# Performance work log

Hardware: AMD Instinct MI355X
Metric: run time of the kernel (lower is better)

Reference implementation:

```python
import jax, jax.numpy as jnp
import numpy as np
import math

H, NH, DH, FF = 768, 12, 64, 3072
B, S = 8, 1024

def _gelu(x):
    return x * 0.5 * (1.0 + jax.lax.erf(x / math.sqrt(2.0)))

def _layernorm(x, gamma, beta, eps=1e-6):
    mean = jnp.mean(x, axis=-1, keepdims=True)
    std = jnp.std(x, axis=-1, keepdims=True, ddof=1)  # torch unbiased std
    return gamma * (x - mean) / (std + eps) + beta

def setup_inputs() -> dict:
    key = jax.random.key(0)
    ks = jax.random.split(key, 16)
    p = lambda k, shape: jax.random.normal(k, shape, dtype=jnp.float32) * 0.02
    return {
        "hidden": jax.random.normal(ks[0], (B, S, H), dtype=jnp.float32),
        "mask": jnp.zeros((B, 1, S, S), dtype=jnp.float32),
        "position_bias": jax.random.normal(ks[1], (1, NH, S, S), dtype=jnp.float32),
        "Wq": p(ks[2], (H, H)), "bq": jnp.zeros((H,), jnp.float32),
        "Wk": p(ks[3], (H, H)), "bk": jnp.zeros((H,), jnp.float32),
        "Wv": p(ks[4], (H, H)), "bv": jnp.zeros((H,), jnp.float32),
        "Wo": p(ks[5], (H, H)), "bo": jnp.zeros((H,), jnp.float32),
        "W1": p(ks[6], (H, FF)), "b1": jnp.zeros((FF,), jnp.float32),
        "W2": p(ks[7], (FF, H)), "b2": jnp.zeros((H,), jnp.float32),
        "g1": jnp.ones((H,), jnp.float32), "beta1": jnp.zeros((H,), jnp.float32),
        "g2": jnp.ones((H,), jnp.float32), "beta2": jnp.zeros((H,), jnp.float32),
    }

def reference(hidden, mask, position_bias, Wq, bq, Wk, bk, Wv, bv, Wo, bo,
              W1, b1, W2, b2, g1, beta1, g2, beta2):
    b, s, _ = hidden.shape
    def split_heads(x):
        return x.reshape(b, s, NH, DH).transpose(0, 2, 1, 3)  # [b, h, s, d]
    q = split_heads(hidden @ Wq + bq)
    k = split_heads(hidden @ Wk + bk)
    v = split_heads(hidden @ Wv + bv)
    scores = jnp.einsum('bhqd,bhkd->bhqk', q, k)
    scores = scores + position_bias          # bias added BEFORE scaling (as in source)
    scores = scores / math.sqrt(float(DH))
    scores = scores + mask
    probs = jax.nn.softmax(scores, axis=-1)  # dropout is identity in eval
    ctx = jnp.einsum('bhqk,bhkd->bhqd', probs, v)
    ctx = ctx.transpose(0, 2, 1, 3).reshape(b, s, NH * DH)
    attn_out = ctx @ Wo + bo
    inter = _layernorm(attn_out + hidden, g1, beta1)
    ffn = _gelu(inter @ W1 + b1) @ W2 + b2
    return _layernorm(ffn + inter, g2, beta2)
```

## Files before the change

### kernel.cpp

```cpp
#include <hip/hip_runtime.h>
#include <cmath>

typedef __bf16 bf16;
typedef __attribute__((ext_vector_type(8))) __bf16 bf16x8;
typedef __attribute__((ext_vector_type(4))) __bf16 bf16x4;
typedef __attribute__((ext_vector_type(4))) float f32x4;

#define DEVINL __device__ __forceinline__

DEVINL void gload16(const void* g, void* l) {
    __builtin_amdgcn_global_load_lds((const __attribute__((address_space(1))) void*)g,
                                     (__attribute__((address_space(3))) void*)l, 16, 0, 0);
}


__global__ void cast_bf16_kernel(const float* __restrict__ in, bf16* __restrict__ out, int n4) {
    int i = blockIdx.x * 256 + threadIdx.x;
    if (i < n4) {
        float4 v = ((const float4*)in)[i];
        bf16x4 o;
        o[0] = (bf16)v.x; o[1] = (bf16)v.y; o[2] = (bf16)v.z; o[3] = (bf16)v.w;
        ((bf16x4*)out)[i] = o;
    }
}

__global__ void prep_pm_kernel(const float* __restrict__ pb, const float* __restrict__ mask,
                               bf16* __restrict__ pbs, bf16* __restrict__ maskb,
                               int n1, int n2) {
    const int i = blockIdx.x * 256 + threadIdx.x;
    const float c1 = 0.18033688011112042f;
    const float c2 = 1.4426950408889634f;
    if (i < n1) {
        float4 v = ((const float4*)pb)[i];
        bf16x4 o;
        o[0] = (bf16)(v.x * c1); o[1] = (bf16)(v.y * c1);
        o[2] = (bf16)(v.z * c1); o[3] = (bf16)(v.w * c1);
        ((bf16x4*)pbs)[i] = o;
    } else if (i < n1 + n2) {
        const int j = i - n1;
        float4 v = ((const float4*)mask)[j];
        bf16x4 o;
        o[0] = (bf16)(v.x * c2); o[1] = (bf16)(v.y * c2);
        o[2] = (bf16)(v.z * c2); o[3] = (bf16)(v.w * c2);
        ((bf16x4*)maskb)[j] = o;
    }
}

__global__ void tcast_kernel(const float* __restrict__ in, bf16* __restrict__ out, int R, int C) {
    __shared__ float t[32][33];
    int tx = threadIdx.x & 31, ty = threadIdx.x >> 5;
    int r0 = blockIdx.y * 32, c0 = blockIdx.x * 32;
#pragma unroll
    for (int i = 0; i < 4; ++i)
        t[ty + 8 * i][tx] = in[(size_t)(r0 + ty + 8 * i) * C + c0 + tx];
    __syncthreads();
#pragma unroll
    for (int i = 0; i < 4; ++i)
        out[(size_t)(c0 + ty + 8 * i) * R + r0 + tx] = (bf16)t[tx][ty + 8 * i];
}

__global__ void concat_bias_kernel(const float* __restrict__ a, const float* __restrict__ b,
                                   const float* __restrict__ c, float* __restrict__ out) {
    int i = blockIdx.x * 256 + threadIdx.x;
    if (i < 2304) out[i] = (i < 768) ? a[i] : ((i < 1536) ? b[i - 768] : c[i - 1536]);
}

__global__ __launch_bounds__(256) void vtrans_kernel(const bf16* __restrict__ qkv,
                                                     bf16* __restrict__ vT) {
    __shared__ bf16 t[64][72];
    const int tid = threadIdx.x;
    const int bh = blockIdx.y, s0 = blockIdx.x * 32;
    const int b = bh / 12, h = bh % 12;
    {
        const int r = tid >> 3, c8 = (tid & 7) * 8;
        bf16x8 v = *(const bf16x8*)(qkv + (size_t)(b * 1024 + s0 + r) * 2304 + 1536 + h * 64 + c8);
#pragma unroll
        for (int j = 0; j < 8; ++j) t[c8 + j][r] = v[j];
    }
    __syncthreads();
    {
        const int d = tid >> 2, s8 = (tid & 3) * 8;
        bf16x8 o = *(const bf16x8*)(&t[d][s8]);
        *(bf16x8*)(vT + (size_t)(bh * 64 + d) * 1024 + s0 + s8) = o;
    }
}

template<int MODE, int BN>
__global__ __launch_bounds__(256, 4) void gemm_kernel(const bf16* __restrict__ A, const bf16* __restrict__ Bt,
                                                      const float* __restrict__ bias,
                                                      bf16* __restrict__ Cb,
                                                      int M, int N, int K, int ldc) {
    constexpr int NI = BN / 32;
    constexpr int BLOADS = BN / 32;
    __shared__ __align__(16) bf16 As[128 * 64];
    __shared__ __align__(16) bf16 Bs[BN * 64];
    const int tid = threadIdx.x;
    const int wid = tid >> 6, lane = tid & 63;
    const int L = blockIdx.y * gridDim.x + blockIdx.x;
    const int cpx = (gridDim.x * gridDim.y) >> 3;
    const int wg = (L & 7) * cpx + (L >> 3);
    const int m0 = (wg / gridDim.x) * 128, n0 = (wg % gridDim.x) * BN;
    const int wr = (wid >> 1) * 64, wc = (wid & 1) * (BN / 2);
    const int lg = lane >> 4, l15 = lane & 15;
    f32x4 acc[4][NI] = {};

    for (int k0 = 0; k0 < K; k0 += 64) {
        __syncthreads();
#pragma unroll
        for (int i = 0; i < 4; ++i) {
            const int cbase = (wid * 4 + i) * 1024;
            const int td = cbase + lane * 16;
            const int row = td >> 7;
            const int s16 = ((td >> 4) & 7) ^ (row & 7);
            gload16(A + (size_t)(m0 + row) * K + k0 + s16 * 8, (char*)As + cbase);
        }
#pragma unroll
        for (int i = 0; i < BLOADS; ++i) {
            const int cbase = (wid * BLOADS + i) * 1024;
            const int td = cbase + lane * 16;
            const int row = td >> 7;
            const int s16 = ((td >> 4) & 7) ^ (row & 7);
            gload16(Bt + (size_t)(n0 + row) * K + k0 + s16 * 8, (char*)Bs + cbase);
        }
        __syncthreads();
#pragma unroll
        for (int kk = 0; kk < 2; ++kk) {
            bf16x8 af[4], bfr[NI];
#pragma unroll
            for (int mi = 0; mi < 4; ++mi) {
                int ra = wr + mi * 16 + l15;
                int off = (ra * 128 + (kk * 32 + 8 * lg) * 2) ^ ((ra & 7) << 4);
                af[mi] = *(const bf16x8*)((const char*)As + off);
            }
#pragma unroll
            for (int ni = 0; ni < NI; ++ni) {
                int rb = wc + ni * 16 + l15;
                int off = (rb * 128 + (kk * 32 + 8 * lg) * 2) ^ ((rb & 7) << 4);
                bfr[ni] = *(const bf16x8*)((const char*)Bs + off);
            }
#pragma unroll
            for (int mi = 0; mi < 4; ++mi)
#pragma unroll
                for (int ni = 0; ni < NI; ++ni)
                    acc[mi][ni] = __builtin_amdgcn_mfma_f32_16x16x32_bf16(af[mi], bfr[ni], acc[mi][ni], 0, 0, 0);
        }
    }
#pragma unroll
    for (int mi = 0; mi < 4; ++mi) {
#pragma unroll
        for (int r = 0; r < 4; ++r) {
            const int row = m0 + wr + mi * 16 + lg * 4 + r;
#pragma unroll
            for (int ni = 0; ni < NI; ++ni) {
                const int col = n0 + wc + ni * 16 + l15;
                float v = acc[mi][ni][r] + bias[col];
                if (MODE == 2) v = v * 0.5f * (1.0f + erff(v * 0.70710678118654752f));
                Cb[(size_t)row * ldc + col] = (bf16)v;
            }
        }
    }
}

__global__ __launch_bounds__(256, 3) void attn_kernel(const bf16* __restrict__ qkv,
                                                      const bf16* __restrict__ pbs,
                                                      const bf16* __restrict__ maskb,
                                                      const bf16* __restrict__ vT,
                                                      bf16* __restrict__ ctx) {
    __shared__ __align__(16) bf16 Kb[3][64 * 64];
    __shared__ __align__(16) bf16 Vb[3][64 * 64];
    const int tid = threadIdx.x, wid = tid >> 6, lane = tid & 63;
    const int bh = blockIdx.y, b = bh / 12, h = bh % 12;
    const int q0 = blockIdx.x * 128 + wid * 32;
    const int lg = lane >> 4, l15 = lane & 15;
    const float cqk = 0.18033688011112042f;

    bf16x8 aq[2][2];
#pragma unroll
    for (int qs = 0; qs < 2; ++qs) {
        const size_t r = (size_t)(b * 1024 + q0 + qs * 16 + l15) * 2304 + h * 64 + 8 * lg;
        aq[qs][0] = *(const bf16x8*)(qkv + r);
        aq[qs][1] = *(const bf16x8*)(qkv + r + 32);
    }

    auto stage = [&](int tt, int pp) {
#pragma unroll
        for (int rd = 0; rd < 2; ++rd) {
            const int n = rd * 256 + tid;
            const int i = n >> 3, sl = n & 7, c = sl ^ (i & 7);
            const int sig = (i & 32) | ((i & 12) << 1) | ((i & 16) >> 2) | (i & 3);
            gload16(qkv + (size_t)(b * 1024 + tt * 64 + sig) * 2304 + 768 + h * 64 + c * 8,
                    (char*)Kb[pp] + (rd * 256 + wid * 64) * 16);
            gload16(vT + ((size_t)bh * 64 + i) * 1024 + tt * 64 + c * 8,
                    (char*)Vb[pp] + (rd * 256 + wid * 64) * 16);
        }
    };

    float mrun[2] = {-1e30f, -1e30f}, lsum[2] = {0.f, 0.f};
    f32x4 acc[2][4] = {};

    stage(0, 0);
    stage(1, 1);
    __syncthreads();
    for (int t = 0; t < 16; ++t) {
        const int p = t % 3;
        const int k0 = t * 64;
        bf16x8 pbv[2][2], mkv[2][2];
#pragma unroll
        for (int qs = 0; qs < 2; ++qs) {
            const int q = q0 + qs * 16 + l15;
            const bf16* pr = pbs + ((size_t)h * 1024 + q) * 1024 + k0 + lg * 8;
            const bf16* mr = maskb + ((size_t)b * 1024 + q) * 1024 + k0 + lg * 8;
            pbv[qs][0] = *(const bf16x8*)pr;  pbv[qs][1] = *(const bf16x8*)(pr + 32);
            mkv[qs][0] = *(const bf16x8*)mr;  mkv[qs][1] = *(const bf16x8*)(mr + 32);
        }
        if (t < 14) stage(t + 2, (t + 2) % 3);

        bf16x8 bk[4][2];
#pragma unroll
        for (int kt = 0; kt < 4; ++kt) {
            const int row = kt * 16 + l15;
            const int byte = (row * 128 + lg * 16) ^ ((row & 7) << 4);
            bk[kt][0] = *(const bf16x8*)((const char*)Kb[p] + byte);
            bk[kt][1] = *(const bf16x8*)((const char*)Kb[p] + (byte ^ 64));
        }
        f32x4 s[2][4];
#pragma unroll
        for (int qs = 0; qs < 2; ++qs)
#pragma unroll
            for (int kt = 0; kt < 4; ++kt) {
                f32x4 z = {};
                z = __builtin_amdgcn_mfma_f32_16x16x32_bf16(bk[kt][0], aq[qs][0], z, 0, 0, 0);
                z = __builtin_amdgcn_mfma_f32_16x16x32_bf16(bk[kt][1], aq[qs][1], z, 0, 0, 0);
                s[qs][kt] = z;
            }
#pragma unroll
        for (int qs = 0; qs < 2; ++qs)
#pragma unroll
            for (int kt = 0; kt < 4; ++kt)
#pragma unroll
                for (int r = 0; r < 4; ++r) {
                    const int j = (kt & 1) * 4 + r;
                    s[qs][kt][r] = s[qs][kt][r] * cqk
                                 + (float)pbv[qs][kt >> 1][j]
                                 + (float)mkv[qs][kt >> 1][j];
                }
        bf16x8 po[2][2];
#pragma unroll
        for (int qs = 0; qs < 2; ++qs) {
            float tm = s[qs][0][0];
#pragma unroll
            for (int kt = 0; kt < 4; ++kt)
#pragma unroll
                for (int r = 0; r < 4; ++r) tm = fmaxf(tm, s[qs][kt][r]);
            tm = fmaxf(tm, __shfl_xor(tm, 16));
            tm = fmaxf(tm, __shfl_xor(tm, 32));
            if (!__all(tm <= mrun[qs] + 6.0f)) {
                const float mn = fmaxf(mrun[qs], tm);
                const float scal = __builtin_amdgcn_exp2f(mrun[qs] - mn);
                mrun[qs] = mn;
                lsum[qs] *= scal;
#pragma unroll
                for (int dt = 0; dt < 4; ++dt) {
                    acc[qs][dt][0] *= scal; acc[qs][dt][1] *= scal;
                    acc[qs][dt][2] *= scal; acc[qs][dt][3] *= scal;
                }
            }
            float ts = 0.f;
#pragma unroll
            for (int kt = 0; kt < 4; ++kt)
#pragma unroll
                for (int r = 0; r < 4; ++r) {
                    const float pv = __builtin_amdgcn_exp2f(s[qs][kt][r] - mrun[qs]);
                    ts += pv;
                    const int idx = kt * 4 + r;
                    if (idx < 8) po[qs][0][idx] = (bf16)pv;
                    else         po[qs][1][idx - 8] = (bf16)pv;
                }
            ts += __shfl_xor(ts, 16);
            ts += __shfl_xor(ts, 32);
            lsum[qs] += ts;
        }
        bf16x8 vb[4][2];
#pragma unroll
        for (int dt = 0; dt < 4; ++dt) {
            const int row = dt * 16 + l15;
            const int byte = (row * 128 + lg * 16) ^ ((row & 7) << 4);
            vb[dt][0] = *(const bf16x8*)((const char*)Vb[p] + byte);
            vb[dt][1] = *(const bf16x8*)((const char*)Vb[p] + (byte ^ 64));
        }
#pragma unroll
        for (int qs = 0; qs < 2; ++qs)
#pragma unroll
            for (int dt = 0; dt < 4; ++dt) {
                acc[qs][dt] = __builtin_amdgcn_mfma_f32_16x16x32_bf16(vb[dt][0], po[qs][0], acc[qs][dt], 0, 0, 0);
                acc[qs][dt] = __builtin_amdgcn_mfma_f32_16x16x32_bf16(vb[dt][1], po[qs][1], acc[qs][dt], 0, 0, 0);
            }
        __syncthreads();
    }
    char* scr = (char*)Kb + wid * 4096;
#pragma unroll
    for (int qs = 0; qs < 2; ++qs) {
        const float inv = 1.0f / lsum[qs];
        const int ql = qs * 16 + l15;
#pragma unroll
        for (int dt = 0; dt < 4; ++dt) {
            bf16x4 o;
#pragma unroll
            for (int r = 0; r < 4; ++r) o[r] = (bf16)(acc[qs][dt][r] * inv);
            const int wb = (ql * 128 + dt * 32 + lg * 8) ^ ((ql & 7) << 4);
            *(bf16x4*)(scr + wb) = o;
        }
    }
    __syncthreads();
#pragma unroll
    for (int qs = 0; qs < 2; ++qs) {
        const int ql = qs * 16 + l15;
        const int rb = (ql * 128 + lg * 32) ^ ((ql & 7) << 4);
        bf16x8 o0 = *(const bf16x8*)(scr + rb);
        bf16x8 o1 = *(const bf16x8*)(scr + (rb ^ 16));
        bf16* cp = ctx + (size_t)(b * 1024 + q0 + ql) * 768 + h * 64 + lg * 16;
        *(bf16x8*)cp = o0;
        *(bf16x8*)(cp + 8) = o1;
    }
}

template<int MODE>
__global__ __launch_bounds__(256) void ln_kernel(const bf16* __restrict__ xb,
                                                 const float* __restrict__ resf,
                                                 const bf16* __restrict__ resb,
                                                 const float* __restrict__ g, const float* __restrict__ bt,
                                                 float* __restrict__ outf, bf16* __restrict__ outb) {
    const int wid = threadIdx.x >> 6, lane = threadIdx.x & 63;
    const int row = blockIdx.x * 4 + wid;
    float4 v[3];
    float s = 0.f, ss = 0.f;
#pragma unroll
    for (int j = 0; j < 3; ++j) {
        bf16x4 xa = ((const bf16x4*)(xb + (size_t)row * 768))[lane + 64 * j];
        float4 b;
        if (MODE == 0) {
            b = ((const float4*)(resf + (size_t)row * 768))[lane + 64 * j];
        } else {
            bf16x4 rb = ((const bf16x4*)(resb + (size_t)row * 768))[lane + 64 * j];
            b.x = (float)rb[0]; b.y = (float)rb[1]; b.z = (float)rb[2]; b.w = (float)rb[3];
        }
        float4 w;
        w.x = (float)xa[0] + b.x; w.y = (float)xa[1] + b.y;
        w.z = (float)xa[2] + b.z; w.w = (float)xa[3] + b.w;
        v[j] = w;
        s += w.x + w.y + w.z + w.w;
        ss += w.x * w.x + w.y * w.y + w.z * w.z + w.w * w.w;
    }
#pragma unroll
    for (int off = 1; off <= 32; off <<= 1) { s += __shfl_xor(s, off); ss += __shfl_xor(ss, off); }
    const float mean = s * (1.f / 768.f);
    float var = (ss - 768.f * mean * mean) * (1.f / 767.f);
    var = fmaxf(var, 0.f);
    const float inv = 1.f / (sqrtf(var) + 1e-6f);
#pragma unroll
    for (int j = 0; j < 3; ++j) {
        float4 gv = ((const float4*)g)[lane + 64 * j];
        float4 bv = ((const float4*)bt)[lane + 64 * j];
        float4 y;
        y.x = gv.x * (v[j].x - mean) * inv + bv.x;
        y.y = gv.y * (v[j].y - mean) * inv + bv.y;
        y.z = gv.z * (v[j].z - mean) * inv + bv.z;
        y.w = gv.w * (v[j].w - mean) * inv + bv.w;
        if (MODE == 1) {
            ((float4*)(outf + (size_t)row * 768))[lane + 64 * j] = y;
        } else {
            bf16x4 o;
            o[0] = (bf16)y.x; o[1] = (bf16)y.y; o[2] = (bf16)y.z; o[3] = (bf16)y.w;
            ((bf16x4*)(outb + (size_t)row * 768))[lane + 64 * j] = o;
        }
    }
}


extern "C" void kernel_launch(void* const* d_in, const int* in_sizes, int n_in,
                              void* d_out, int out_size, void* d_ws, size_t ws_size,
                              hipStream_t stream) {
    const float* hidden = (const float*)d_in[0];
    const float* mask   = (const float*)d_in[1];
    const float* pb     = (const float*)d_in[2];
    const float* Wq = (const float*)d_in[3];
    const float* bq = (const float*)d_in[4];
    const float* Wk = (const float*)d_in[5];
    const float* bk = (const float*)d_in[6];
    const float* Wv = (const float*)d_in[7];
    const float* bv = (const float*)d_in[8];
    const float* Wo = (const float*)d_in[9];
    const float* bo = (const float*)d_in[10];
    const float* W1 = (const float*)d_in[11];
    const float* b1 = (const float*)d_in[12];
    const float* W2 = (const float*)d_in[13];
    const float* b2 = (const float*)d_in[14];
    const float* g1  = (const float*)d_in[15];
    const float* be1 = (const float*)d_in[16];
    const float* g2  = (const float*)d_in[17];
    const float* be2 = (const float*)d_in[18];
    float* out = (float*)d_out;

    char* ws = (char*)d_ws;
    bf16*  xbf      = (bf16*)(ws);
    bf16*  wqkv_t   = (bf16*)(ws + 12582912);
    bf16*  wo_t     = (bf16*)(ws + 16121856);
    bf16*  w1_t     = (bf16*)(ws + 17301504);
    bf16*  w2_t     = (bf16*)(ws + 22020096);
    float* bqkv     = (float*)(ws + 26738688);
    bf16*  qkv      = (bf16*)(ws + 26747904);
    bf16*  ffn1     = qkv;
    bf16*  vT       = (bf16*)(ws + 26747904 + 37748736);
    bf16*  ctx      = (bf16*)(ws + 77079552);
    bf16*  pbs      = (bf16*)(ws + 89662464);
    bf16*  attn_outb= (bf16*)(ws + 89662464);
    bf16*  maskb    = (bf16*)(ws + 114828288);
    bf16*  ffn2b    = (bf16*)(ws + 114828288);
    bf16*  interb   = xbf;

    cast_bf16_kernel<<<6291456 / 4 / 256, 256, 0, stream>>>(hidden, xbf, 6291456 / 4);
    tcast_kernel<<<dim3(24, 24), 256, 0, stream>>>(Wq, wqkv_t, 768, 768);
    tcast_kernel<<<dim3(24, 24), 256, 0, stream>>>(Wk, wqkv_t + 768 * 768, 768, 768);
    tcast_kernel<<<dim3(24, 24), 256, 0, stream>>>(Wv, wqkv_t + 2 * 768 * 768, 768, 768);
    tcast_kernel<<<dim3(24, 24), 256, 0, stream>>>(Wo, wo_t, 768, 768);
    tcast_kernel<<<dim3(96, 24), 256, 0, stream>>>(W1, w1_t, 768, 3072);
    tcast_kernel<<<dim3(24, 96), 256, 0, stream>>>(W2, w2_t, 3072, 768);
    concat_bias_kernel<<<9, 256, 0, stream>>>(bq, bk, bv, bqkv);
    prep_pm_kernel<<<(3145728 + 2097152) / 256, 256, 0, stream>>>(pb, mask, pbs, maskb,
                                                                  3145728, 2097152);

    gemm_kernel<0, 128><<<dim3(18, 64), 256, 0, stream>>>(xbf, wqkv_t, bqkv, qkv, 8192, 2304, 768, 2304);
    vtrans_kernel<<<dim3(32, 96), 256, 0, stream>>>(qkv, vT);
    attn_kernel<<<dim3(8, 96), 256, 0, stream>>>(qkv, pbs, maskb, vT, ctx);
    gemm_kernel<0, 64><<<dim3(12, 64), 256, 0, stream>>>(ctx, wo_t, bo, attn_outb, 8192, 768, 768, 768);
    ln_kernel<0><<<2048, 256, 0, stream>>>(attn_outb, hidden, nullptr, g1, be1, nullptr, interb);
    gemm_kernel<2, 128><<<dim3(24, 64), 256, 0, stream>>>(interb, w1_t, b1, ffn1, 8192, 3072, 768, 3072);
    gemm_kernel<0, 64><<<dim3(12, 64), 256, 0, stream>>>(ffn1, w2_t, b2, ffn2b, 8192, 768, 3072, 768);
    ln_kernel<1><<<2048, 256, 0, stream>>>(ffn2b, nullptr, interb, g2, be2, out, nullptr);
}
```

Baseline: 311.1 us.

## Compute V transposed directly via swapped GEMM and relax attention barriers

Splits the fused QKV projection into a QK GEMM and a separate V GEMM that computes Wv^T·x^T, so it writes V directly in the per-head transposed layout the attention kernel reads. This removes the vtrans kernel and its extra pass over V. The attention loop also replaces __syncthreads with a partial vmcnt wait plus s_barrier, so in-flight prefetches are not fully drained, and raises wave priority around the MFMA blocks. The transposed-store epilogue scatters bf16 writes with stride 1024, which may coalesce worse than the original row-major store.

```diff
diff --git a/kernel.cpp b/kernel.cpp
--- a/kernel.cpp
+++ b/kernel.cpp
@@ -60,29 +60,9 @@
 }
 
 __global__ void concat_bias_kernel(const float* __restrict__ a, const float* __restrict__ b,
-                                   const float* __restrict__ c, float* __restrict__ out) {
+                                   float* __restrict__ out) {
     int i = blockIdx.x * 256 + threadIdx.x;
-    if (i < 2304) out[i] = (i < 768) ? a[i] : ((i < 1536) ? b[i - 768] : c[i - 1536]);
-}
-
-__global__ __launch_bounds__(256) void vtrans_kernel(const bf16* __restrict__ qkv,
-                                                     bf16* __restrict__ vT) {
-    __shared__ bf16 t[64][72];
-    const int tid = threadIdx.x;
-    const int bh = blockIdx.y, s0 = blockIdx.x * 32;
-    const int b = bh / 12, h = bh % 12;
-    {
-        const int r = tid >> 3, c8 = (tid & 7) * 8;
-        bf16x8 v = *(const bf16x8*)(qkv + (size_t)(b * 1024 + s0 + r) * 2304 + 1536 + h * 64 + c8);
-#pragma unroll
-        for (int j = 0; j < 8; ++j) t[c8 + j][r] = v[j];
-    }
-    __syncthreads();
-    {
-        const int d = tid >> 2, s8 = (tid & 3) * 8;
-        bf16x8 o = *(const bf16x8*)(&t[d][s8]);
-        *(bf16x8*)(vT + (size_t)(bh * 64 + d) * 1024 + s0 + s8) = o;
-    }
+    if (i < 1536) out[i] = (i < 768) ? a[i] : b[i - 768];
 }
 
 template<int MODE, int BN>
@@ -153,15 +133,18 @@
 #pragma unroll
             for (int ni = 0; ni < NI; ++ni) {
                 const int col = n0 + wc + ni * 16 + l15;
-                float v = acc[mi][ni][r] + bias[col];
+                float v = acc[mi][ni][r] + bias[(MODE == 3) ? row : col];
                 if (MODE == 2) v = v * 0.5f * (1.0f + erff(v * 0.70710678118654752f));
-                Cb[(size_t)row * ldc + col] = (bf16)v;
-            }
-        }
-    }
-}
-
-__global__ __launch_bounds__(256, 3) void attn_kernel(const bf16* __restrict__ qkv,
+                if (MODE == 3)
+                    Cb[((size_t)(col >> 10) * 768 + row) * 1024 + (col & 1023)] = (bf16)v;
+                else
+                    Cb[(size_t)row * ldc + col] = (bf16)v;
+            }
+        }
+    }
+}
+
+__global__ __launch_bounds__(256, 3) void attn_kernel(const bf16* __restrict__ qk,
                                                       const bf16* __restrict__ pbs,
                                                       const bf16* __restrict__ maskb,
                                                       const bf16* __restrict__ vT,
@@ -177,9 +160,9 @@
     bf16x8 aq[2][2];
 #pragma unroll
     for (int qs = 0; qs < 2; ++qs) {
-        const size_t r = (size_t)(b * 1024 + q0 + qs * 16 + l15) * 2304 + h * 64 + 8 * lg;
-        aq[qs][0] = *(const bf16x8*)(qkv + r);
-        aq[qs][1] = *(const bf16x8*)(qkv + r + 32);
+        const size_t r = (size_t)(b * 1024 + q0 + qs * 16 + l15) * 1536 + h * 64 + 8 * lg;
+        aq[qs][0] = *(const bf16x8*)(qk + r);
+        aq[qs][1] = *(const bf16x8*)(qk + r + 32);
     }
 
     auto stage = [&](int tt, int pp) {
@@ -188,7 +171,7 @@
             const int n = rd * 256 + tid;
             const int i = n >> 3, sl = n & 7, c = sl ^ (i & 7);
             const int sig = (i & 32) | ((i & 12) << 1) | ((i & 16) >> 2) | (i & 3);
-            gload16(qkv + (size_t)(b * 1024 + tt * 64 + sig) * 2304 + 768 + h * 64 + c * 8,
+            gload16(qk + (size_t)(b * 1024 + tt * 64 + sig) * 1536 + 768 + h * 64 + c * 8,
                     (char*)Kb[pp] + (rd * 256 + wid * 64) * 16);
             gload16(vT + ((size_t)bh * 64 + i) * 1024 + tt * 64 + c * 8,
                     (char*)Vb[pp] + (rd * 256 + wid * 64) * 16);
@@ -200,7 +183,8 @@
 
     stage(0, 0);
     stage(1, 1);
-    __syncthreads();
+    asm volatile("s_waitcnt vmcnt(4)" ::: "memory");
+    __builtin_amdgcn_s_barrier();
     for (int t = 0; t < 16; ++t) {
         const int p = t % 3;
         const int k0 = t * 64;
@@ -224,6 +208,7 @@
             bk[kt][1] = *(const bf16x8*)((const char*)Kb[p] + (byte ^ 64));
         }
         f32x4 s[2][4];
+        __builtin_amdgcn_s_setprio(1);
 #pragma unroll
         for (int qs = 0; qs < 2; ++qs)
 #pragma unroll
@@ -233,6 +218,7 @@
                 z = __builtin_amdgcn_mfma_f32_16x16x32_bf16(bk[kt][1], aq[qs][1], z, 0, 0, 0);
                 s[qs][kt] = z;
             }
+        __builtin_amdgcn_s_setprio(0);
 #pragma unroll
         for (int qs = 0; qs < 2; ++qs)
 #pragma unroll
@@ -288,6 +274,7 @@
             vb[dt][0] = *(const bf16x8*)((const char*)Vb[p] + byte);
             vb[dt][1] = *(const bf16x8*)((const char*)Vb[p] + (byte ^ 64));
         }
+        __builtin_amdgcn_s_setprio(1);
 #pragma unroll
         for (int qs = 0; qs < 2; ++qs)
 #pragma unroll
@@ -295,7 +282,9 @@
                 acc[qs][dt] = __builtin_amdgcn_mfma_f32_16x16x32_bf16(vb[dt][0], po[qs][0], acc[qs][dt], 0, 0, 0);
                 acc[qs][dt] = __builtin_amdgcn_mfma_f32_16x16x32_bf16(vb[dt][1], po[qs][1], acc[qs][dt], 0, 0, 0);
             }
-        __syncthreads();
+        __builtin_amdgcn_s_setprio(0);
+        asm volatile("s_waitcnt vmcnt(4)" ::: "memory");
+        __builtin_amdgcn_s_barrier();
     }
     char* scr = (char*)Kb + wid * 4096;
 #pragma unroll
@@ -407,31 +396,32 @@
     bf16*  wo_t     = (bf16*)(ws + 16121856);
     bf16*  w1_t     = (bf16*)(ws + 17301504);
     bf16*  w2_t     = (bf16*)(ws + 22020096);
-    float* bqkv     = (float*)(ws + 26738688);
-    bf16*  qkv      = (bf16*)(ws + 26747904);
-    bf16*  ffn1     = qkv;
-    bf16*  vT       = (bf16*)(ws + 26747904 + 37748736);
+    float* bqk      = (float*)(ws + 26738688);
+    bf16*  qk       = (bf16*)(ws + 26747904);
+    bf16*  ffn1     = qk;
+    bf16*  vT       = (bf16*)(ws + 26747904 + 25165824);
     bf16*  ctx      = (bf16*)(ws + 77079552);
     bf16*  pbs      = (bf16*)(ws + 89662464);
     bf16*  attn_outb= (bf16*)(ws + 89662464);
     bf16*  maskb    = (bf16*)(ws + 114828288);
     bf16*  ffn2b    = (bf16*)(ws + 114828288);
     bf16*  interb   = xbf;
+    bf16*  wv_t     = wqkv_t + 2 * 768 * 768;
 
     cast_bf16_kernel<<<6291456 / 4 / 256, 256, 0, stream>>>(hidden, xbf, 6291456 / 4);
     tcast_kernel<<<dim3(24, 24), 256, 0, stream>>>(Wq, wqkv_t, 768, 768);
     tcast_kernel<<<dim3(24, 24), 256, 0, stream>>>(Wk, wqkv_t + 768 * 768, 768, 768);
-    tcast_kernel<<<dim3(24, 24), 256, 0, stream>>>(Wv, wqkv_t + 2 * 768 * 768, 768, 768);
+    tcast_kernel<<<dim3(24, 24), 256, 0, stream>>>(Wv, wv_t, 768, 768);
     tcast_kernel<<<dim3(24, 24), 256, 0, stream>>>(Wo, wo_t, 768, 768);
     tcast_kernel<<<dim3(96, 24), 256, 0, stream>>>(W1, w1_t, 768, 3072);
     tcast_kernel<<<dim3(24, 96), 256, 0, stream>>>(W2, w2_t, 3072, 768);
-    concat_bias_kernel<<<9, 256, 0, stream>>>(bq, bk, bv, bqkv);
+    concat_bias_kernel<<<6, 256, 0, stream>>>(bq, bk, bqk);
     prep_pm_kernel<<<(3145728 + 2097152) / 256, 256, 0, stream>>>(pb, mask, pbs, maskb,
                                                                   3145728, 2097152);
 
-    gemm_kernel<0, 128><<<dim3(18, 64), 256, 0, stream>>>(xbf, wqkv_t, bqkv, qkv, 8192, 2304, 768, 2304);
-    vtrans_kernel<<<dim3(32, 96), 256, 0, stream>>>(qkv, vT);
-    attn_kernel<<<dim3(8, 96), 256, 0, stream>>>(qkv, pbs, maskb, vT, ctx);
+    gemm_kernel<0, 128><<<dim3(12, 64), 256, 0, stream>>>(xbf, wqkv_t, bqk, qk, 8192, 1536, 768, 1536);
+    gemm_kernel<3, 128><<<dim3(64, 6), 256, 0, stream>>>(wv_t, xbf, bv, vT, 768, 8192, 768, 0);
+    attn_kernel<<<dim3(8, 96), 256, 0, stream>>>(qk, pbs, maskb, vT, ctx);
     gemm_kernel<0, 64><<<dim3(12, 64), 256, 0, stream>>>(ctx, wo_t, bo, attn_outb, 8192, 768, 768, 768);
     ln_kernel<0><<<2048, 256, 0, stream>>>(attn_outb, hidden, nullptr, g1, be1, nullptr, interb);
     gemm_kernel<2, 128><<<dim3(24, 64), 256, 0, stream>>>(interb, w1_t, b1, ffn1, 8192, 3072, 768, 3072);
```

Result: no change. 305.8 us (-1.7%).
